# Performance work log

Hardware: AMD Instinct MI355X
Metric: run time of the kernel (lower is better)

## Reference

```python
import jax, jax.numpy as jnp
import numpy as np

DIM = 256
HEADS = 8
DIM_HEAD = 64
EPS = 1e-12  # F.normalize eps


def rms_norm(x, w, dim):
    # F.normalize over channel dim (axis=1) * weight * sqrt(dim)
    n = jnp.sqrt(jnp.sum(x * x, axis=1, keepdims=True))
    xn = x / jnp.maximum(n, EPS)
    return xn * w[None, :, None, None] * (dim ** 0.5)


def setup_inputs() -> dict:
    key = jax.random.key(0)
    ks = jax.random.split(key, 4)
    hd = HEADS * DIM_HEAD
    return {
        "x": jax.random.normal(ks[0], (16, DIM, 64, 64), dtype=jnp.float32),
        "norm_w": jnp.ones((DIM,), jnp.float32),
        "qkv_w": jax.random.normal(ks[1], (3 * hd, DIM), jnp.float32) * (DIM ** -0.5),
        "out_w": jax.random.normal(ks[2], (DIM, hd), jnp.float32) * (hd ** -0.5),
        "out_b": jnp.zeros((DIM,), jnp.float32),
        "out_norm_w": jnp.ones((DIM,), jnp.float32),
    }


def reference(x, norm_w, qkv_w, out_w, out_b, out_norm_w):
    b, c, H, W = x.shape
    n = H * W
    scale = DIM_HEAD ** -0.5

    xn = rms_norm(x, norm_w, DIM)
    # 1x1 conv == channel matmul: [3hd, c] x [b, c, H, W]
    qkv = jnp.einsum('oc,bchw->bohw', qkv_w, xn)
    q, k, v = jnp.split(qkv, 3, axis=1)

    def to_heads(t):
        # b (h d) x y -> b h d n
        return t.reshape(b, HEADS, DIM_HEAD, n)

    q = jax.nn.softmax(to_heads(q), axis=2) * scale  # softmax over feature dim d
    k = jax.nn.softmax(to_heads(k), axis=3)          # softmax over spatial n
    v = to_heads(v)

    ctx = jnp.einsum('bhdn,bhen->bhde', k, v)   # [b,h,d,e]
    out = jnp.einsum('bhde,bhdn->bhen', ctx, q) # [b,h,e,n]
    out = out.reshape(b, HEADS * DIM_HEAD, H, W)

    out = jnp.einsum('oc,bchw->bohw', out_w, out) + out_b[None, :, None, None]
    return rms_norm(out, out_norm_w, DIM)
```

## Files before the change

kernel.cpp:

```cpp
#include <hip/hip_runtime.h>

#define C_ 256
#define N_ 4096
#define NH_ 8

typedef unsigned short u16;
typedef unsigned int u32;
typedef __attribute__((ext_vector_type(8))) short s8v;
typedef __attribute__((ext_vector_type(4))) float f4v;

#define MFMA16 __builtin_amdgcn_mfma_f32_16x16x32_bf16

__device__ __forceinline__ float bf2f(u16 b){ union{u32 u; float f;} v; v.u=((u32)b)<<16; return v.f; }
__device__ __forceinline__ u16 f2bf(float f){ union{float f; u32 u;} v; v.f=f; return (u16)((v.u + 0x7FFFu + ((v.u>>16)&1u))>>16); }

__device__ __forceinline__ void gl_lds16(const u16* g, u16* l){
  __builtin_amdgcn_global_load_lds((const __attribute__((address_space(1))) u32*)g,
                                   (__attribute__((address_space(3))) u32*)l, 16, 0, 0);
}

__global__ __launch_bounds__(256) void k_prep(const float* __restrict__ x, const float* __restrict__ nw,
                                              u16* __restrict__ xnT){
  __shared__ float red[256];
  __shared__ float nws[256];
  const int tid = threadIdx.x;
  nws[tid] = nw[tid];
  const int blk = blockIdx.x, b = blk>>6, n0 = (blk&63)*64;
  const int cq = tid>>6, px = tid&63;
  const float* xp = x + (size_t)b*(C_*N_) + (size_t)(cq*64)*N_ + n0 + px;
  float v[64]; float s = 0.f;
  #pragma unroll
  for (int i=0;i<64;i++){ float t = xp[(size_t)i*N_]; v[i]=t; s = fmaf(t,t,s); }
  red[tid] = s;
  __syncthreads();
  const float st = red[px] + red[64+px] + red[128+px] + red[192+px];
  const float r = 16.0f / fmaxf(sqrtf(st), 1e-12f);
  u16* o = xnT + ((size_t)b*4096 + n0 + px)*256 + cq*64;
  #pragma unroll
  for (int i=0;i<64;i+=2){
    *(u32*)(o+i) = (u32)f2bf(v[i]*r*nws[cq*64+i]) | ((u32)f2bf(v[i+1]*r*nws[cq*64+i+1])<<16);
  }
}

__global__ __launch_bounds__(256) void k_wconv(const float* __restrict__ qkvw, const float* __restrict__ ow,
                                               u16* __restrict__ wqkv, u16* __restrict__ owb){
  int q = blockIdx.x*256 + threadIdx.x;
  int i = q*4;
  const float4 f4 = (i < 393216) ? *(const float4*)&qkvw[i] : *(const float4*)&ow[i-393216];
  u32 lo = (u32)f2bf(f4.x) | ((u32)f2bf(f4.y)<<16);
  u32 hi = (u32)f2bf(f4.z) | ((u32)f2bf(f4.w)<<16);
  u16* dst = (i < 393216) ? (wqkv + i) : (owb + (i-393216));
  *(u32*)dst = lo;
  *(u32*)(dst+2) = hi;
}

__global__ __launch_bounds__(256,3) void k_kv(const u16* __restrict__ xnT, const u16* __restrict__ wqkv,
    u16* __restrict__ ctxp, float* __restrict__ Mp, float* __restrict__ Sp){
  __shared__ u16 xs[64*256];
  __shared__ u16 pbuf[64*72];
  __shared__ u16 vbuf[64*72];
  const int idx = blockIdx.x;
  const int ch = idx&7, h = (idx>>3)&7, b = idx>>6;
  const int tid=threadIdx.x, w=tid>>6, l=tid&63, l15=l&15, lg=l>>4;
  const int swl = (l15&7)<<4;
  const u16* xb  = xnT + (size_t)b*(4096*256);
  const int srow = (l>>5);
  const int scolB = (l&31)*16;
  s8v ak[8], av[8];
  {
    const u16* wkp = wqkv + (size_t)(512 + h*64 + w*16 + l15)*256 + lg*8;
    #pragma unroll
    for (int cs=0; cs<8; cs++){ ak[cs] = *(const s8v*)(wkp + cs*32); av[cs] = *(const s8v*)(wkp + 131072 + cs*32); }
  }
  int colOff[8];
  #pragma unroll
  for (int cs=0; cs<8; cs++) colOff[cs] = (((cs<<6)+(lg<<4)) ^ swl)>>1;

  f4v acc[4];
  #pragma unroll
  for (int et=0;et<4;et++) acc[et] = (f4v){0.f,0.f,0.f,0.f};
  float ps[4] = {0.f,0.f,0.f,0.f};

  {
    const int n0 = ch*512;
    #pragma unroll
    for (int i=0;i<8;i++){
      int rloc = w*16 + i*2 + srow;
      int scol = scolB ^ ((rloc&7)<<4);
      gl_lds16(xb + (size_t)(n0+rloc)*256 + (scol>>1), &xs[(w*16+i*2)*256]);
    }
  }

  for (int t=0; t<8; ++t){
    __syncthreads();
    f4v kacc[4], vacc[4];
    #pragma unroll
    for (int ns=0;ns<4;ns++){ kacc[ns]=(f4v){0.f,0.f,0.f,0.f}; vacc[ns]=(f4v){0.f,0.f,0.f,0.f}; }
    #pragma unroll
    for (int cs=0; cs<8; cs++){
      #pragma unroll
      for (int ns=0; ns<4; ns++){
        s8v bfr = *(const s8v*)&xs[(ns*16+l15)*256 + colOff[cs]];
        kacc[ns] = MFMA16(ak[cs], bfr, kacc[ns], 0,0,0);
        vacc[ns] = MFMA16(av[cs], bfr, vacc[ns], 0,0,0);
      }
    }
    #pragma unroll
    for (int j=0;j<4;j++){
      const int row = w*16 + lg*4 + j;
      #pragma unroll
      for (int ns=0;ns<4;ns++){
        float e = __expf(kacc[ns][j] - 30.0f);
        ps[j] += e;
        pbuf[row*72 + ns*16+l15] = f2bf(e);
        vbuf[row*72 + ns*16+l15] = f2bf(vacc[ns][j]);
      }
    }
    __syncthreads();
    if (t<7){
      const int n0 = ch*512 + (t+1)*64;
      #pragma unroll
      for (int i=0;i<8;i++){
        int rloc = w*16 + i*2 + srow;
        int scol = scolB ^ ((rloc&7)<<4);
        gl_lds16(xb + (size_t)(n0+rloc)*256 + (scol>>1), &xs[(w*16+i*2)*256]);
      }
    }
    #pragma unroll
    for (int ks=0; ks<2; ks++){
      s8v af = *(const s8v*)(pbuf + (w*16+l15)*72 + ks*32 + lg*8);
      #pragma unroll
      for (int et=0; et<4; et++){
        s8v bv = *(const s8v*)(vbuf + (et*16+l15)*72 + ks*32 + lg*8);
        acc[et] = MFMA16(af, bv, acc[et], 0,0,0);
      }
    }
  }
  u16* cp = ctxp + (((size_t)ch*16 + b)*8 + h)*4096;
  #pragma unroll
  for (int et=0; et<4; et++)
    #pragma unroll
    for (int j=0;j<4;j++)
      cp[(w*16+lg*4+j)*64 + et*16+l15] = f2bf(acc[et][j]);
  #pragma unroll
  for (int j=0;j<4;j++){
    float s = ps[j];
    s += __shfl_xor(s,1); s += __shfl_xor(s,2);
    s += __shfl_xor(s,4); s += __shfl_xor(s,8);
    ps[j] = s;
  }
  if (l15==0){
    #pragma unroll
    for (int j=0;j<4;j++){
      int rg = (b*8+h)*64 + w*16 + lg*4 + j;
      Mp[ch*8192+rg]=30.0f; Sp[ch*8192+rg]=ps[j];
    }
  }
}

__global__ __launch_bounds__(256) void k_comb(const u16* __restrict__ ctxp, const float* __restrict__ Mp,
    const float* __restrict__ Sp, u16* __restrict__ ctxT){
  __shared__ float fs[8][64];
  __shared__ float iSs[64];
  const int bh = blockIdx.x, tid = threadIdx.x;
  if (tid < 64){
    float m[8];
    float Mg = -1e30f;
    #pragma unroll
    for (int ch=0;ch<8;ch++){ m[ch] = Mp[ch*8192 + bh*64 + tid]; Mg = fmaxf(Mg, m[ch]); }
    float Sg = 0.f;
    #pragma unroll
    for (int ch=0;ch<8;ch++){
      float fv = __expf(m[ch]-Mg);
      fs[ch][tid] = fv;
      Sg += Sp[ch*8192 + bh*64 + tid]*fv;
    }
    iSs[tid] = 1.0f / Sg;
  }
  __syncthreads();
  const int e = tid>>2, d0 = (tid&3)*16;
  u16* op = ctxT + (size_t)bh*4096 + e*64 + d0;
  #pragma unroll
  for (int i=0;i<16;i++){
    int d = d0+i;
    float v = 0.f;
    #pragma unroll
    for (int ch=0;ch<8;ch++)
      v += bf2f(ctxp[((size_t)(ch*128)+bh)*4096 + d*64 + e]) * fs[ch][d];
    op[i] = f2bf(v * iSs[d]);
  }
}

__global__ __launch_bounds__(512,2) void k_qout(const u16* __restrict__ xnT, const u16* __restrict__ wqkv,
    const u16* __restrict__ owb, const u16* __restrict__ ctxT,
    const float* __restrict__ ob, const float* __restrict__ onw, float* __restrict__ out){
  __shared__ u16 WQ[64*256];
  __shared__ u16 OWs[256*64];
  __shared__ u16 qa[8][1024];
  const int tid = threadIdx.x;
  const int w=tid>>6, l=tid&63, l15=l&15, lg=l>>4;
  const int blk=blockIdx.x, b=blk>>5, n0=(blk&31)*128 + w*16;
  const u16* xb = xnT + ((size_t)b*4096 + n0)*256;
  const u16* cxb0 = ctxT + ((size_t)b*8)*4096;
  u16* qaw = qa[w];
  const int wqRow0 = (l>>5);
  const int wqColB = (l&31)*16;
  const int owRow0 = (l>>3);
  const int owColB = (l&7)*16;
  s8v ax[8];
  #pragma unroll
  for (int cs=0;cs<8;cs++) ax[cs] = *(const s8v*)(xb + (size_t)l15*256 + cs*32 + lg*8);
  f4v oacc[16];
  #pragma unroll
  for (int mt=0;mt<16;mt++) oacc[mt] = (f4v){0.f,0.f,0.f,0.f};

  #pragma unroll
  for (int i=0;i<4;i++){
    int row = (i*8+w)*2 + wqRow0;
    int scol = wqColB ^ ((row&15)<<4);
    gl_lds16(wqkv + (size_t)row*256 + (scol>>1), &WQ[(i*8+w)*512]);
  }
  #pragma unroll
  for (int i=0;i<4;i++){
    int row = (i*8+w)*8 + owRow0;
    int scol = owColB ^ ((row&7)<<4);
    gl_lds16(owb + (size_t)row*512 + (scol>>1), &OWs[(i*8+w)*512]);
  }

  for (int h=0; h<8; ++h){
    __syncthreads();
    s8v bc[8];
    {
      const u16* cxb = cxb0 + (size_t)h*4096;
      #pragma unroll
      for (int ks=0; ks<2; ks++)
        #pragma unroll
        for (int et=0; et<4; et++)
          bc[ks*4+et] = *(const s8v*)(cxb + (et*16+l15)*64 + ks*32 + lg*8);
    }
    if (h>0){
      #pragma unroll
      for (int i=0;i<4;i++){
        int row = (i*8+w)*8 + owRow0;
        int scol = owColB ^ ((row&7)<<4);
        gl_lds16(owb + (size_t)row*512 + h*64 + (scol>>1), &OWs[(i*8+w)*512]);
      }
    }
    f4v qacc[4];
    #pragma unroll
    for (int dt=0;dt<4;dt++) qacc[dt] = (f4v){0.f,0.f,0.f,0.f};
    #pragma unroll
    for (int dt=0; dt<4; dt++){
      #pragma unroll
      for (int cs=0; cs<8; cs++){
        s8v bw = *(const s8v*)&WQ[(dt*16+l15)*256 + ((((cs<<6)|(lg<<4)) ^ (l15<<4))>>1)];
        qacc[dt] = MFMA16(ax[cs], bw, qacc[dt], 0,0,0);
      }
    }
    #pragma unroll
    for (int j=0;j<4;j++){
      float m = fmaxf(fmaxf(qacc[0][j],qacc[1][j]),fmaxf(qacc[2][j],qacc[3][j]));
      #pragma unroll
      for (int d=1; d<16; d<<=1) m = fmaxf(m, __shfl_xor(m, d));
      float s = 0.f;
      #pragma unroll
      for (int dt=0;dt<4;dt++){ float e=__expf(qacc[dt][j]-m); qacc[dt][j]=e; s+=e; }
      #pragma unroll
      for (int d=1; d<16; d<<=1) s += __shfl_xor(s, d);
      float inv = 0.125f/s;
      #pragma unroll
      for (int dt=0;dt<4;dt++){
        int row = lg*4+j;
        qaw[((row<<6) + dt*16 + l15) ^ ((row&7)<<3)] = f2bf(qacc[dt][j]*inv);
      }
    }
    f4v aacc[4];
    #pragma unroll
    for (int et=0;et<4;et++) aacc[et] = (f4v){0.f,0.f,0.f,0.f};
    #pragma unroll
    for (int ks=0; ks<2; ks++){
      s8v aq = *(const s8v*)&qaw[(l15<<6) + ((((ks<<6)|(lg<<4)) ^ ((l15&7)<<4))>>1)];
      #pragma unroll
      for (int et=0; et<4; et++)
        aacc[et] = MFMA16(aq, bc[ks*4+et], aacc[et], 0,0,0);
    }
    #pragma unroll
    for (int et=0;et<4;et++)
      #pragma unroll
      for (int j=0;j<4;j++){
        int row = lg*4+j;
        qaw[((row<<6) + et*16 + l15) ^ ((row&7)<<3)] = f2bf(aacc[et][j]);
      }
    __syncthreads();
    if (h<7){
      const u16* wqg = wqkv + (size_t)(h+1)*64*256;
      #pragma unroll
      for (int i=0;i<4;i++){
        int row = (i*8+w)*2 + wqRow0;
        int scol = wqColB ^ ((row&15)<<4);
        gl_lds16(wqg + (size_t)row*256 + (scol>>1), &WQ[(i*8+w)*512]);
      }
    }
    #pragma unroll
    for (int ks=0; ks<2; ks++){
      s8v ba = *(const s8v*)&qaw[(l15<<6) + ((((ks<<6)|(lg<<4)) ^ ((l15&7)<<4))>>1)];
      #pragma unroll
      for (int mt=0; mt<16; mt++){
        s8v aw = *(const s8v*)&OWs[(mt*16+l15)*64 + ((((ks<<6)|(lg<<4)) ^ ((l15&7)<<4))>>1)];
        oacc[mt] = MFMA16(aw, ba, oacc[mt], 0,0,0);
      }
    }
  }
  float ss = 0.f;
  #pragma unroll
  for (int mt=0;mt<16;mt++){
    const float4 o4 = *(const float4*)&ob[mt*16 + lg*4];
    #pragma unroll
    for (int j=0;j<4;j++){
      float v = oacc[mt][j] + ((const float*)&o4)[j];
      oacc[mt][j] = v;
      ss = fmaf(v,v,ss);
    }
  }
  ss += __shfl_xor(ss, 16);
  ss += __shfl_xor(ss, 32);
  const float r = 16.0f / fmaxf(sqrtf(ss), 1e-12f);
  float* op = out + (size_t)b*(256*4096) + n0 + l15;
  #pragma unroll
  for (int mt=0;mt<16;mt++){
    const float4 w4 = *(const float4*)&onw[mt*16 + lg*4];
    #pragma unroll
    for (int j=0;j<4;j++){
      int cout = mt*16+lg*4+j;
      op[(size_t)cout*4096] = oacc[mt][j] * r * ((const float*)&w4)[j];
    }
  }
}

extern "C" void kernel_launch(void* const* d_in, const int* in_sizes, int n_in,
                              void* d_out, int out_size, void* d_ws, size_t ws_size,
                              hipStream_t stream){
  const float* x    = (const float*)d_in[0];
  const float* nw   = (const float*)d_in[1];
  const float* qkvw = (const float*)d_in[2];
  const float* ow   = (const float*)d_in[3];
  const float* ob   = (const float*)d_in[4];
  const float* onw  = (const float*)d_in[5];
  float* out = (float*)d_out;
  char* ws = (char*)d_ws;
  u16*   xnT  = (u16*)(ws);
  u16*   wqkv = (u16*)(ws + 33554432);
  u16*   owb  = (u16*)(ws + 34340864);
  u16*   ctxT = (u16*)(ws + 34603008);
  u16*   ctxp = (u16*)(ws + 35651584);
  float* Mp   = (float*)(ws + 44040192);
  float* Sp   = (float*)(ws + 44302336);
  (void)in_sizes; (void)n_in; (void)out_size; (void)ws_size;

  k_wconv<<<512, 256, 0, stream>>>(qkvw, ow, wqkv, owb);
  k_prep <<<1024, 256, 0, stream>>>(x, nw, xnT);
  k_kv   <<<1024, 256, 0, stream>>>(xnT, wqkv, ctxp, Mp, Sp);
  k_comb <<<128, 256, 0, stream>>>(ctxp, Mp, Sp, ctxT);
  k_qout <<<512, 512, 0, stream>>>(xnT, wqkv, owb, ctxT, ob, onw, out);
}
```

Baseline: 177.9 us.

## Fold out-projection weights into per-head context matrix and double-buffer LDS loads

```diff
diff --git a/kernel.cpp b/kernel.cpp
--- a/kernel.cpp
+++ b/kernel.cpp
@@ -159,7 +159,7 @@
 }
 
 __global__ __launch_bounds__(256) void k_comb(const u16* __restrict__ ctxp, const float* __restrict__ Mp,
-    const float* __restrict__ Sp, u16* __restrict__ ctxT){
+    const float* __restrict__ Sp, u16* __restrict__ ctxD){
   __shared__ float fs[8][64];
   __shared__ float iSs[64];
   const int bh = blockIdx.x, tid = threadIdx.x;
@@ -178,35 +178,72 @@
     iSs[tid] = 1.0f / Sg;
   }
   __syncthreads();
-  const int e = tid>>2, d0 = (tid&3)*16;
-  u16* op = ctxT + (size_t)bh*4096 + e*64 + d0;
+  const int d = tid>>2, e0 = (tid&3)*16;
+  u16* op = ctxD + (size_t)bh*4096 + d*64 + e0;
+  const float fsc = iSs[d];
   #pragma unroll
   for (int i=0;i<16;i++){
-    int d = d0+i;
     float v = 0.f;
     #pragma unroll
     for (int ch=0;ch<8;ch++)
-      v += bf2f(ctxp[((size_t)(ch*128)+bh)*4096 + d*64 + e]) * fs[ch][d];
-    op[i] = f2bf(v * iSs[d]);
-  }
+      v += bf2f(ctxp[(size_t)ch*524288 + (size_t)bh*4096 + d*64 + e0+i]) * fs[ch][d];
+    op[i] = f2bf(v * fsc);
+  }
+}
+
+__global__ __launch_bounds__(256) void k_g(const u16* __restrict__ owb, const u16* __restrict__ ctxD,
+                                           u16* __restrict__ G){
+  const int bh = blockIdx.x, h = bh&7;
+  const int tid = threadIdx.x, w = tid>>6, l = tid&63, l15 = l&15, lg = l>>4;
+  s8v a[4][2], bD[4][2];
+  #pragma unroll
+  for (int mt=0; mt<4; mt++)
+    #pragma unroll
+    for (int ks=0; ks<2; ks++)
+      a[mt][ks] = *(const s8v*)(owb + (size_t)(w*64+mt*16+l15)*512 + h*64 + ks*32 + lg*8);
+  #pragma unroll
+  for (int dt=0; dt<4; dt++)
+    #pragma unroll
+    for (int ks=0; ks<2; ks++)
+      bD[dt][ks] = *(const s8v*)(ctxD + (size_t)bh*4096 + (dt*16+l15)*64 + ks*32 + lg*8);
+  f4v acc[4][4];
+  #pragma unroll
+  for (int mt=0;mt<4;mt++)
+    #pragma unroll
+    for (int dt=0;dt<4;dt++) acc[mt][dt] = (f4v){0.f,0.f,0.f,0.f};
+  #pragma unroll
+  for (int ks=0; ks<2; ks++)
+    #pragma unroll
+    for (int mt=0; mt<4; mt++)
+      #pragma unroll
+      for (int dt=0; dt<4; dt++)
+        acc[mt][dt] = MFMA16(a[mt][ks], bD[dt][ks], acc[mt][dt], 0,0,0);
+  u16* gp = G + (size_t)bh*16384;
+  #pragma unroll
+  for (int mt=0; mt<4; mt++)
+    #pragma unroll
+    for (int dt=0; dt<4; dt++)
+      #pragma unroll
+      for (int j=0; j<4; j++)
+        gp[(w*64 + mt*16 + lg*4 + j)*64 + dt*16 + l15] = f2bf(acc[mt][dt][j]);
 }
 
 __global__ __launch_bounds__(512,2) void k_qout(const u16* __restrict__ xnT, const u16* __restrict__ wqkv,
-    const u16* __restrict__ owb, const u16* __restrict__ ctxT,
-    const float* __restrict__ ob, const float* __restrict__ onw, float* __restrict__ out){
-  __shared__ u16 WQ[64*256];
-  __shared__ u16 OWs[256*64];
+    const u16* __restrict__ Gg, const float* __restrict__ ob, const float* __restrict__ onw,
+    float* __restrict__ out){
+  __shared__ u16 WQb[2][64*256];
+  __shared__ u16 Gb[2][256*64];
   __shared__ u16 qa[8][1024];
   const int tid = threadIdx.x;
   const int w=tid>>6, l=tid&63, l15=l&15, lg=l>>4;
   const int blk=blockIdx.x, b=blk>>5, n0=(blk&31)*128 + w*16;
   const u16* xb = xnT + ((size_t)b*4096 + n0)*256;
-  const u16* cxb0 = ctxT + ((size_t)b*8)*4096;
+  const u16* Gbase = Gg + (size_t)b*8*16384;
   u16* qaw = qa[w];
   const int wqRow0 = (l>>5);
   const int wqColB = (l&31)*16;
-  const int owRow0 = (l>>3);
-  const int owColB = (l&7)*16;
+  const int gRow0  = (l>>3);
+  const int gColB  = (l&7)*16;
   s8v ax[8];
   #pragma unroll
   for (int cs=0;cs<8;cs++) ax[cs] = *(const s8v*)(xb + (size_t)l15*256 + cs*32 + lg*8);
@@ -218,32 +255,32 @@
   for (int i=0;i<4;i++){
     int row = (i*8+w)*2 + wqRow0;
     int scol = wqColB ^ ((row&15)<<4);
-    gl_lds16(wqkv + (size_t)row*256 + (scol>>1), &WQ[(i*8+w)*512]);
+    gl_lds16(wqkv + (size_t)row*256 + (scol>>1), &WQb[0][(i*8+w)*512]);
   }
   #pragma unroll
   for (int i=0;i<4;i++){
-    int row = (i*8+w)*8 + owRow0;
-    int scol = owColB ^ ((row&7)<<4);
-    gl_lds16(owb + (size_t)row*512 + (scol>>1), &OWs[(i*8+w)*512]);
+    int row = (i*8+w)*8 + gRow0;
+    int scol = gColB ^ ((row&7)<<4);
+    gl_lds16(Gbase + (size_t)row*64 + (scol>>1), &Gb[0][(i*8+w)*512]);
   }
 
   for (int h=0; h<8; ++h){
+    const int p = h&1;
     __syncthreads();
-    s8v bc[8];
-    {
-      const u16* cxb = cxb0 + (size_t)h*4096;
-      #pragma unroll
-      for (int ks=0; ks<2; ks++)
-        #pragma unroll
-        for (int et=0; et<4; et++)
-          bc[ks*4+et] = *(const s8v*)(cxb + (et*16+l15)*64 + ks*32 + lg*8);
-    }
-    if (h>0){
+    if (h<7){
+      const u16* wqg = wqkv + (size_t)(h+1)*64*256;
+      const u16* gg  = Gbase + (size_t)(h+1)*16384;
       #pragma unroll
       for (int i=0;i<4;i++){
-        int row = (i*8+w)*8 + owRow0;
-        int scol = owColB ^ ((row&7)<<4);
-        gl_lds16(owb + (size_t)row*512 + h*64 + (scol>>1), &OWs[(i*8+w)*512]);
+        int row = (i*8+w)*2 + wqRow0;
+        int scol = wqColB ^ ((row&15)<<4);
+        gl_lds16(wqg + (size_t)row*256 + (scol>>1), &WQb[p^1][(i*8+w)*512]);
+      }
+      #pragma unroll
+      for (int i=0;i<4;i++){
+        int row = (i*8+w)*8 + gRow0;
+        int scol = gColB ^ ((row&7)<<4);
+        gl_lds16(gg + (size_t)row*64 + (scol>>1), &Gb[p^1][(i*8+w)*512]);
       }
     }
     f4v qacc[4];
@@ -253,7 +290,7 @@
     for (int dt=0; dt<4; dt++){
       #pragma unroll
       for (int cs=0; cs<8; cs++){
-        s8v bw = *(const s8v*)&WQ[(dt*16+l15)*256 + ((((cs<<6)|(lg<<4)) ^ (l15<<4))>>1)];
+        s8v bw = *(const s8v*)&WQb[p][(dt*16+l15)*256 + ((((cs<<6)|(lg<<4)) ^ (l15<<4))>>1)];
         qacc[dt] = MFMA16(ax[cs], bw, qacc[dt], 0,0,0);
       }
     }
@@ -274,39 +311,12 @@
         qaw[((row<<6) + dt*16 + l15) ^ ((row&7)<<3)] = f2bf(qacc[dt][j]*inv);
       }
     }
-    f4v aacc[4];
-    #pragma unroll
-    for (int et=0;et<4;et++) aacc[et] = (f4v){0.f,0.f,0.f,0.f};
-    #pragma unroll
-    for (int ks=0; ks<2; ks++){
-      s8v aq = *(const s8v*)&qaw[(l15<<6) + ((((ks<<6)|(lg<<4)) ^ ((l15&7)<<4))>>1)];
-      #pragma unroll
-      for (int et=0; et<4; et++)
-        aacc[et] = MFMA16(aq, bc[ks*4+et], aacc[et], 0,0,0);
-    }
-    #pragma unroll
-    for (int et=0;et<4;et++)
-      #pragma unroll
-      for (int j=0;j<4;j++){
-        int row = lg*4+j;
-        qaw[((row<<6) + et*16 + l15) ^ ((row&7)<<3)] = f2bf(aacc[et][j]);
-      }
-    __syncthreads();
-    if (h<7){
-      const u16* wqg = wqkv + (size_t)(h+1)*64*256;
-      #pragma unroll
-      for (int i=0;i<4;i++){
-        int row = (i*8+w)*2 + wqRow0;
-        int scol = wqColB ^ ((row&15)<<4);
-        gl_lds16(wqg + (size_t)row*256 + (scol>>1), &WQ[(i*8+w)*512]);
-      }
-    }
     #pragma unroll
     for (int ks=0; ks<2; ks++){
       s8v ba = *(const s8v*)&qaw[(l15<<6) + ((((ks<<6)|(lg<<4)) ^ ((l15&7)<<4))>>1)];
       #pragma unroll
       for (int mt=0; mt<16; mt++){
-        s8v aw = *(const s8v*)&OWs[(mt*16+l15)*64 + ((((ks<<6)|(lg<<4)) ^ ((l15&7)<<4))>>1)];
+        s8v aw = *(const s8v*)&Gb[p][(mt*16+l15)*64 + ((((ks<<6)|(lg<<4)) ^ ((l15&7)<<4))>>1)];
         oacc[mt] = MFMA16(aw, ba, oacc[mt], 0,0,0);
       }
     }
@@ -351,8 +361,9 @@
   u16*   xnT  = (u16*)(ws);
   u16*   wqkv = (u16*)(ws + 33554432);
   u16*   owb  = (u16*)(ws + 34340864);
-  u16*   ctxT = (u16*)(ws + 34603008);
+  u16*   ctxD = (u16*)(ws + 34603008);
   u16*   ctxp = (u16*)(ws + 35651584);
+  u16*   G    = ctxp;
   float* Mp   = (float*)(ws + 44040192);
   float* Sp   = (float*)(ws + 44302336);
   (void)in_sizes; (void)n_in; (void)out_size; (void)ws_size;
@@ -360,6 +371,7 @@
   k_wconv<<<512, 256, 0, stream>>>(qkvw, ow, wqkv, owb);
   k_prep <<<1024, 256, 0, stream>>>(x, nw, xnT);
   k_kv   <<<1024, 256, 0, stream>>>(xnT, wqkv, ctxp, Mp, Sp);
-  k_comb <<<128, 256, 0, stream>>>(ctxp, Mp, Sp, ctxT);
-  k_qout <<<512, 512, 0, stream>>>(xnT, wqkv, owb, ctxT, ob, onw, out);
-}
+  k_comb <<<128, 256, 0, stream>>>(ctxp, Mp, Sp, ctxD);
+  k_g    <<<128, 256, 0, stream>>>(owb, ctxD, G);
+  k_qout <<<512, 512, 0, stream>>>(xnT, wqkv, G, ob, onw, out);
+}
```

Measured after the change: 162.2 us. -8.8%, faster.
